# Performance work log

Hardware: AMD Instinct MI355X
Metric: run time of the kernel (lower is better)

Reference implementation:

```python
import jax, jax.numpy as jnp
import numpy as np

B, LQ, LK = 16, 256, 256
DQ = DK = DV = H = 256


def setup_inputs() -> dict:
    key = jax.random.key(0)
    ks = jax.random.split(key, 7)
    queries = jax.random.normal(ks[0], (B, LQ, DQ), dtype=jnp.float32)
    keys = jax.random.normal(ks[1], (B, LK, DK), dtype=jnp.float32)
    values = jax.random.normal(ks[2], (B, LK, DV), dtype=jnp.float32)
    valid_lens = jax.random.randint(ks[3], (B,), 1, LK + 1).astype(jnp.int32)
    W_q = jax.random.normal(ks[4], (DQ, H), dtype=jnp.float32) / np.sqrt(DQ)
    W_k = jax.random.normal(ks[5], (DK, H), dtype=jnp.float32) / np.sqrt(DK)
    w_v = jax.random.normal(ks[6], (H,), dtype=jnp.float32) / np.sqrt(H)
    return {"queries": queries, "keys": keys, "values": values,
            "valid_lens": valid_lens, "W_q": W_q, "W_k": W_k, "w_v": w_v}


def reference(queries, keys, values, valid_lens, W_q, W_k, w_v):
    # Project queries and keys to the hidden size (no bias)
    q = jnp.einsum('bqd,dh->bqh', queries, W_q)          # (B, Lq, H)
    k = jnp.einsum('bkd,dh->bkh', keys, W_k)             # (B, Lk, H)
    # Broadcast-add, tanh, then contract with w_v -> scores (B, Lq, Lk)
    features = jnp.tanh(q[:, :, None, :] + k[:, None, :, :])  # (B, Lq, Lk, H)
    scores = jnp.einsum('bqkh,h->bqk', features, w_v)
    # Masked softmax over last axis: positions >= valid_len get -1e6
    mask = jnp.arange(scores.shape[-1]) < valid_lens[:, None, None]  # (B,1,Lk) bcast
    scores = jnp.where(mask, scores, jnp.float32(-1e6))
    attn = jax.nn.softmax(scores, axis=-1)
    # Dropout is identity at inference (training=False)
    return jnp.einsum('bqk,bkv->bqv', attn, values)      # (B, Lq, Dv)
```

## Files before the change

### kernel.cpp

```cpp
#include <hip/hip_runtime.h>

using bf16x8 = __attribute__((ext_vector_type(8))) __bf16;
using f32x4  = __attribute__((ext_vector_type(4))) float;
using f32x2  = __attribute__((ext_vector_type(2))) float;
using us8    = __attribute__((ext_vector_type(8))) unsigned short;

#define TWO_LOG2E 2.8853900817779268f
#define LOG2E 1.4426950408889634f

__device__ __forceinline__ unsigned short f2bf(float x) {
  unsigned int u = __float_as_uint(x);
  u = (u + 0x7fffu + ((u >> 16) & 1u)) >> 16;
  return (unsigned short)u;
}
__device__ __forceinline__ float bf2f(unsigned short h) {
  return __uint_as_float(((unsigned int)h) << 16);
}
__device__ __forceinline__ f32x2 pk_fma(f32x2 a, f32x2 b, f32x2 c) {
  return __builtin_elementwise_fma(a, b, c);
}

__global__ __launch_bounds__(256) void tcast_kernel(
    const float* __restrict__ Wq, const float* __restrict__ Wk,
    const float* __restrict__ vals, const float* __restrict__ wv,
    unsigned short* __restrict__ wt_hi, unsigned short* __restrict__ wt_lo,
    unsigned short* __restrict__ vt_hi, unsigned short* __restrict__ vt_lo,
    float* __restrict__ wv2, float* __restrict__ Wsum) {
  if (blockIdx.x == 0) {
    int t = threadIdx.x;
    wv2[t] = -2.0f * wv[t];
    if (t < 64) {
      float s = wv[t] + wv[t + 64] + wv[t + 128] + wv[t + 192];
#pragma unroll
      for (int off = 1; off < 64; off <<= 1) s += __shfl_xor(s, off, 64);
      if (t == 0) Wsum[0] = s;
    }
  }
  __shared__ float tile[32][33];
  int m = blockIdx.x >> 6;
  int ts = blockIdx.x & 63;
  int R0 = (ts >> 3) << 5, C0 = (ts & 7) << 5;
  const float* src = (m == 0) ? Wq : (m == 1) ? Wk : (vals + ((m - 2) << 16));
  int r = threadIdx.x >> 3, c4 = (threadIdx.x & 7) << 2;
  float4 v = *(const float4*)(src + (R0 + r) * 256 + C0 + c4);
  tile[r][c4] = v.x; tile[r][c4 + 1] = v.y; tile[r][c4 + 2] = v.z; tile[r][c4 + 3] = v.w;
  __syncthreads();
  float o0 = tile[c4 + 0][r], o1 = tile[c4 + 1][r];
  float o2 = tile[c4 + 2][r], o3 = tile[c4 + 3][r];
  unsigned short h0 = f2bf(o0), h1 = f2bf(o1), h2 = f2bf(o2), h3 = f2bf(o3);
  int base = ((m < 2) ? (m << 16) : ((m - 2) << 16)) + (C0 + r) * 256 + R0 + c4;
  unsigned short* dh = (m < 2) ? wt_hi : vt_hi;
  unsigned short* dl = (m < 2) ? wt_lo : vt_lo;
  *(ushort4*)(dh + base) = make_ushort4(h0, h1, h2, h3);
  *(ushort4*)(dl + base) = make_ushort4(f2bf(o0 - bf2f(h0)), f2bf(o1 - bf2f(h1)),
                                        f2bf(o2 - bf2f(h2)), f2bf(o3 - bf2f(h3)));
}

__global__ __launch_bounds__(256, 4) void proj_kernel(
    const float* __restrict__ q, const float* __restrict__ kk,
    const unsigned short* __restrict__ w_hi, const unsigned short* __restrict__ w_lo,
    const int* __restrict__ vlens, float* __restrict__ Rq, float* __restrict__ RkT) {
  int wave = threadIdx.x >> 6, lane = threadIdx.x & 63;
  int mt = (blockIdx.x << 1) + (wave & 1);
  int m0 = mt << 4;
  int g = mt >> 8;
  if (g) {
    int bb = (m0 >> 8) & 15;
    if ((m0 & 255) >= vlens[bb]) return;
  }
  int r = lane & 15, qd = lane >> 4;
  int row = m0 + r;
  const float* A = (g == 0) ? (q + row * 256) : (kk + (row - 4096) * 256);
  bf16x8 ah[8], al[8];
#pragma unroll
  for (int s = 0; s < 8; ++s) {
    const float* p = A + qd * 8 + s * 32;
    float4 f0 = *(const float4*)p;
    float4 f1 = *(const float4*)(p + 4);
    float fv[8] = {f0.x, f0.y, f0.z, f0.w, f1.x, f1.y, f1.z, f1.w};
#pragma unroll
    for (int j = 0; j < 8; ++j) {
      __bf16 h = (__bf16)fv[j];
      ah[s][j] = h;
      al[s][j] = (__bf16)(fv[j] - (float)h);
    }
  }
  int nbase = (blockIdx.y << 6) + ((wave >> 1) << 5);
#pragma unroll
  for (int tI = 0; tI < 2; ++tI) {
    int n0 = nbase + (tI << 4);
    int boff = (g << 16) + (n0 + r) * 256 + qd * 8;
    f32x4 acc = {0.f, 0.f, 0.f, 0.f};
#pragma unroll
    for (int s = 0; s < 8; ++s) {
      bf16x8 bh = *(const bf16x8*)(w_hi + boff + s * 32);
      bf16x8 bl = *(const bf16x8*)(w_lo + boff + s * 32);
      acc = __builtin_amdgcn_mfma_f32_16x16x32_bf16(ah[s], bh, acc, 0, 0, 0);
      acc = __builtin_amdgcn_mfma_f32_16x16x32_bf16(ah[s], bl, acc, 0, 0, 0);
      acc = __builtin_amdgcn_mfma_f32_16x16x32_bf16(al[s], bh, acc, 0, 0, 0);
    }
    f32x4 ex;
#pragma unroll
    for (int i = 0; i < 4; ++i) {
      float l = acc[i] * TWO_LOG2E;
      l = fminf(fmaxf(l, -27.f), 27.f);
      ex[i] = __builtin_amdgcn_exp2f(l);
    }
    if (g == 0) {
#pragma unroll
      for (int i = 0; i < 4; ++i)
        Rq[(m0 + qd * 4 + i) * 256 + n0 + r] = ex[i];
    } else {
      int b = (m0 >> 8) & 15;
      int kloc = (m0 & 255) + qd * 4;
      *(f32x4*)(RkT + (b << 16) + (n0 + r) * 256 + kloc) = ex;
    }
  }
}

__global__ __launch_bounds__(256, 8) void scores_kernel(
    const float* __restrict__ Rq, const float* __restrict__ RkT,
    const float* __restrict__ wv2, const float* __restrict__ Wsum,
    const int* __restrict__ vlens, float* __restrict__ sc) {
  const int b = blockIdx.x;
  const int k0 = blockIdx.y << 5;
  const int vl = vlens[b];
  if (k0 >= vl) return;
  __shared__ __align__(16) float rqs[32 * 76];
  __shared__ __align__(16) float kT[64 * 34];
  const int t = threadIdx.x;
  const int q0 = blockIdx.z << 5;
  const int qrow = (b << 8) + q0;
  const int tq = t >> 4, tk = t & 15;
  const int sr = t >> 3, shb = (t & 7) << 3;
  const int hrow = t >> 2, kq = (t & 3) << 3;
  f32x2 a0 = {0.f, 0.f}, a1 = {0.f, 0.f};

  for (int hc = 0; hc < 4; ++hc) {
    if (hc) __syncthreads();
    const float* gq = Rq + (qrow + sr) * 256 + (hc << 6) + shb;
    *(float4*)(rqs + sr * 76 + shb)     = *(const float4*)gq;
    *(float4*)(rqs + sr * 76 + shb + 4) = *(const float4*)(gq + 4);
    const float* gk = RkT + (b << 16) + ((hc << 6) + hrow) * 256 + k0 + kq;
    *(float4*)(kT + hrow * 34 + kq)     = *(const float4*)gk;
    *(float4*)(kT + hrow * 34 + kq + 4) = *(const float4*)(gk + 4);
    __syncthreads();
#pragma unroll 2
    for (int h = 0; h < 64; h += 4) {
      f32x4 qa = *(const f32x4*)(rqs + tq * 76 + h);
      f32x4 qb = *(const f32x4*)(rqs + (tq + 16) * 76 + h);
      f32x4 wm = *(const f32x4*)(wv2 + (hc << 6) + h);
#pragma unroll
      for (int j = 0; j < 4; ++j) {
        f32x2 rk = *(const f32x2*)(kT + (h + j) * 34 + (tk << 1));
        f32x2 wj = (f32x2)(wm[j]);
        f32x2 d0 = pk_fma(rk, (f32x2)(qa[j]), (f32x2)(1.0f));
        f32x2 d1 = pk_fma(rk, (f32x2)(qb[j]), (f32x2)(1.0f));
        f32x2 r0, r1;
        r0.x = __uint_as_float(0x7EF311C3u - __float_as_uint(d0.x));
        r0.y = __uint_as_float(0x7EF311C3u - __float_as_uint(d0.y));
        r1.x = __uint_as_float(0x7EF311C3u - __float_as_uint(d1.x));
        r1.y = __uint_as_float(0x7EF311C3u - __float_as_uint(d1.y));
        r0 = r0 * pk_fma(-d0, r0, (f32x2)(2.0f));
        r1 = r1 * pk_fma(-d1, r1, (f32x2)(2.0f));
        a0 = pk_fma(r0, wj, a0);
        a1 = pk_fma(r1, wj, a1);
      }
    }
  }
  float ws = Wsum[0];
  a0 += (f32x2)(ws);
  a1 += (f32x2)(ws);
  *(f32x2*)(sc + ((qrow + tq) << 8) + k0 + (tk << 1)) = a0;
  *(f32x2*)(sc + ((qrow + tq + 16) << 8) + k0 + (tk << 1)) = a1;
}

__global__ __launch_bounds__(256) void av_fused_kernel(
    const float* __restrict__ sc, const int* __restrict__ vlens,
    const unsigned short* __restrict__ vhi, const unsigned short* __restrict__ vlo,
    float* __restrict__ out) {
  __shared__ __align__(16) unsigned short athi[16 * 264];
  const int wave = threadIdx.x >> 6, lane = threadIdx.x & 63;
  const int b = blockIdx.x;
  const int nh = blockIdx.y;
  const int m0 = blockIdx.z << 4;
  const int vl = vlens[b];

  {
    int row = (wave << 2) + (lane & 3);
    int c0 = (lane >> 2) << 4;
    const float* srow = sc + ((b << 8) + m0 + row) * 256 + c0;
    float4 x0 = *(const float4*)(srow);
    float4 x1 = *(const float4*)(srow + 4);
    float4 x2 = *(const float4*)(srow + 8);
    float4 x3 = *(const float4*)(srow + 12);
    float p[16] = {x0.x, x0.y, x0.z, x0.w, x1.x, x1.y, x1.z, x1.w,
                   x2.x, x2.y, x2.z, x2.w, x3.x, x3.y, x3.z, x3.w};
#pragma unroll
    for (int i = 0; i < 16; ++i)
      if (c0 + i >= vl) p[i] = -1e6f;
    float mx = p[0];
#pragma unroll
    for (int i = 1; i < 16; ++i) mx = fmaxf(mx, p[i]);
#pragma unroll
    for (int off = 4; off <= 32; off <<= 1) mx = fmaxf(mx, __shfl_xor(mx, off, 64));
    float sm = 0.f;
#pragma unroll
    for (int i = 0; i < 16; ++i) {
      p[i] = __builtin_amdgcn_exp2f((p[i] - mx) * LOG2E);
      sm += p[i];
    }
#pragma unroll
    for (int off = 4; off <= 32; off <<= 1) sm += __shfl_xor(sm, off, 64);
    float rs = __builtin_amdgcn_rcpf(sm);
    us8 vh[2];
#pragma unroll
    for (int i = 0; i < 16; ++i) vh[i >> 3][i & 7] = f2bf(p[i] * rs);
    *(us8*)(athi + row * 264 + c0)     = vh[0];
    *(us8*)(athi + row * 264 + c0 + 8) = vh[1];
  }
  __syncthreads();

  const int r = lane & 15, qd = lane >> 4;
  const int smax = (vl + 31) >> 5;
#pragma unroll
  for (int tI = 0; tI < 2; ++tI) {
    int n0 = (nh << 7) + (wave << 5) + (tI << 4);
    int boff = (b << 16) + (n0 + r) * 256 + qd * 8;
    f32x4 acc = {0.f, 0.f, 0.f, 0.f};
    for (int s = 0; s < smax; ++s) {
      bf16x8 ah = *(const bf16x8*)(athi + r * 264 + qd * 8 + s * 32);
      bf16x8 bh = *(const bf16x8*)(vhi + boff + s * 32);
      bf16x8 bl = *(const bf16x8*)(vlo + boff + s * 32);
      acc = __builtin_amdgcn_mfma_f32_16x16x32_bf16(ah, bh, acc, 0, 0, 0);
      acc = __builtin_amdgcn_mfma_f32_16x16x32_bf16(ah, bl, acc, 0, 0, 0);
    }
#pragma unroll
    for (int i = 0; i < 4; ++i)
      out[(b << 16) + (m0 + qd * 4 + i) * 256 + n0 + r] = acc[i];
  }
}

extern "C" void kernel_launch(void* const* d_in, const int* in_sizes, int n_in,
                              void* d_out, int out_size, void* d_ws, size_t ws_size,
                              hipStream_t stream) {
  const float* queries = (const float*)d_in[0];
  const float* keys    = (const float*)d_in[1];
  const float* values  = (const float*)d_in[2];
  const int*   vlens   = (const int*)d_in[3];
  const float* Wq      = (const float*)d_in[4];
  const float* Wk      = (const float*)d_in[5];
  const float* wv      = (const float*)d_in[6];
  float* out = (float*)d_out;
  char* ws = (char*)d_ws;

  unsigned short* wt_hi = (unsigned short*)(ws + 0);
  unsigned short* wt_lo = (unsigned short*)(ws + 262144);
  unsigned short* vt_hi = (unsigned short*)(ws + 524288);
  unsigned short* vt_lo = (unsigned short*)(ws + 2621440);
  float*          Rq    = (float*)(ws + 4718592);
  float*          RkT   = (float*)(ws + 8912896);
  float*          sc    = (float*)(ws + 13107200);
  float*          wv2   = (float*)(ws + 17301504);
  float*          Wsum  = (float*)(ws + 17302528);

  tcast_kernel<<<1152, 256, 0, stream>>>(Wq, Wk, values, wv,
                                         wt_hi, wt_lo, vt_hi, vt_lo, wv2, Wsum);
  proj_kernel<<<dim3(256, 4), 256, 0, stream>>>(queries, keys, wt_hi, wt_lo,
                                                vlens, Rq, RkT);
  scores_kernel<<<dim3(16, 8, 8), 256, 0, stream>>>(Rq, RkT, wv2, Wsum, vlens, sc);
  av_fused_kernel<<<dim3(16, 2, 16), 256, 0, stream>>>(sc, vlens, vt_hi, vt_lo, out);
}
```

Before: 139.4 us.

## Use persistent scores kernel with atomic work queue over valid tiles

Replaces the 3D scores grid, where blocks past valid_len exit early, with a persistent grid of 512 blocks. The blocks pull compacted (batch, k-tile, q-tile) items from a global atomic counter, using a prefix sum of per-batch tile counts built in tcast_kernel. This targets load imbalance and the cost of launching blocks that do no work under ragged valid lengths. It adds one atomic and two barriers per item, a linear search over batches, and depends on the counter being reset by the earlier kernel.

```diff
diff --git a/kernel.cpp b/kernel.cpp
--- a/kernel.cpp
+++ b/kernel.cpp
@@ -23,9 +23,11 @@
 __global__ __launch_bounds__(256) void tcast_kernel(
     const float* __restrict__ Wq, const float* __restrict__ Wk,
     const float* __restrict__ vals, const float* __restrict__ wv,
+    const int* __restrict__ vlens,
     unsigned short* __restrict__ wt_hi, unsigned short* __restrict__ wt_lo,
     unsigned short* __restrict__ vt_hi, unsigned short* __restrict__ vt_lo,
-    float* __restrict__ wv2, float* __restrict__ Wsum) {
+    float* __restrict__ wv2, float* __restrict__ Wsum,
+    int* __restrict__ ctr, int* __restrict__ cum) {
   if (blockIdx.x == 0) {
     int t = threadIdx.x;
     wv2[t] = -2.0f * wv[t];
@@ -34,6 +36,15 @@
 #pragma unroll
       for (int off = 1; off < 64; off <<= 1) s += __shfl_xor(s, off, 64);
       if (t == 0) Wsum[0] = s;
+    }
+    if (t == 0) {
+      ctr[0] = 0;
+      int c = 0;
+      for (int b = 0; b < 16; ++b) {
+        cum[b] = c;
+        c += ((vlens[b] + 31) >> 5) << 3;
+      }
+      cum[16] = c;
     }
   }
   __shared__ float tile[32][33];
@@ -121,58 +132,69 @@
 __global__ __launch_bounds__(256, 8) void scores_kernel(
     const float* __restrict__ Rq, const float* __restrict__ RkT,
     const float* __restrict__ wv2, const float* __restrict__ Wsum,
-    const int* __restrict__ vlens, float* __restrict__ sc) {
-  const int b = blockIdx.x;
-  const int k0 = blockIdx.y << 5;
-  const int vl = vlens[b];
-  if (k0 >= vl) return;
+    const int* __restrict__ cum, int* __restrict__ ctr,
+    float* __restrict__ sc) {
   __shared__ __align__(16) float rqs[32 * 76];
   __shared__ __align__(16) float kT[64 * 34];
+  __shared__ int s_item;
   const int t = threadIdx.x;
-  const int q0 = blockIdx.z << 5;
-  const int qrow = (b << 8) + q0;
   const int tq = t >> 4, tk = t & 15;
   const int sr = t >> 3, shb = (t & 7) << 3;
   const int hrow = t >> 2, kq = (t & 3) << 3;
-  f32x2 a0 = {0.f, 0.f}, a1 = {0.f, 0.f};
-
-  for (int hc = 0; hc < 4; ++hc) {
-    if (hc) __syncthreads();
-    const float* gq = Rq + (qrow + sr) * 256 + (hc << 6) + shb;
-    *(float4*)(rqs + sr * 76 + shb)     = *(const float4*)gq;
-    *(float4*)(rqs + sr * 76 + shb + 4) = *(const float4*)(gq + 4);
-    const float* gk = RkT + (b << 16) + ((hc << 6) + hrow) * 256 + k0 + kq;
-    *(float4*)(kT + hrow * 34 + kq)     = *(const float4*)gk;
-    *(float4*)(kT + hrow * 34 + kq + 4) = *(const float4*)(gk + 4);
+  const int total = cum[16];
+  const float ws = Wsum[0];
+
+  for (;;) {
     __syncthreads();
+    if (t == 0) s_item = atomicAdd(ctr, 1);
+    __syncthreads();
+    const int w = s_item;
+    if (w >= total) return;
+    int b = 0;
+    while (cum[b + 1] <= w) ++b;
+    const int local = w - cum[b];
+    const int k0 = (local >> 3) << 5;
+    const int q0 = (local & 7) << 5;
+    const int qrow = (b << 8) + q0;
+    f32x2 a0 = {0.f, 0.f}, a1 = {0.f, 0.f};
+
+    for (int hc = 0; hc < 4; ++hc) {
+      if (hc) __syncthreads();
+      const float* gq = Rq + (qrow + sr) * 256 + (hc << 6) + shb;
+      *(float4*)(rqs + sr * 76 + shb)     = *(const float4*)gq;
+      *(float4*)(rqs + sr * 76 + shb + 4) = *(const float4*)(gq + 4);
+      const float* gk = RkT + (b << 16) + ((hc << 6) + hrow) * 256 + k0 + kq;
+      *(float4*)(kT + hrow * 34 + kq)     = *(const float4*)gk;
+      *(float4*)(kT + hrow * 34 + kq + 4) = *(const float4*)(gk + 4);
+      __syncthreads();
 #pragma unroll 2
-    for (int h = 0; h < 64; h += 4) {
-      f32x4 qa = *(const f32x4*)(rqs + tq * 76 + h);
-      f32x4 qb = *(const f32x4*)(rqs + (tq + 16) * 76 + h);
-      f32x4 wm = *(const f32x4*)(wv2 + (hc << 6) + h);
-#pragma unroll
-      for (int j = 0; j < 4; ++j) {
-        f32x2 rk = *(const f32x2*)(kT + (h + j) * 34 + (tk << 1));
-        f32x2 wj = (f32x2)(wm[j]);
-        f32x2 d0 = pk_fma(rk, (f32x2)(qa[j]), (f32x2)(1.0f));
-        f32x2 d1 = pk_fma(rk, (f32x2)(qb[j]), (f32x2)(1.0f));
-        f32x2 r0, r1;
-        r0.x = __uint_as_float(0x7EF311C3u - __float_as_uint(d0.x));
-        r0.y = __uint_as_float(0x7EF311C3u - __float_as_uint(d0.y));
-        r1.x = __uint_as_float(0x7EF311C3u - __float_as_uint(d1.x));
-        r1.y = __uint_as_float(0x7EF311C3u - __float_as_uint(d1.y));
-        r0 = r0 * pk_fma(-d0, r0, (f32x2)(2.0f));
-        r1 = r1 * pk_fma(-d1, r1, (f32x2)(2.0f));
-        a0 = pk_fma(r0, wj, a0);
-        a1 = pk_fma(r1, wj, a1);
+      for (int h = 0; h < 64; h += 4) {
+        f32x4 qa = *(const f32x4*)(rqs + tq * 76 + h);
+        f32x4 qb = *(const f32x4*)(rqs + (tq + 16) * 76 + h);
+        f32x4 wm = *(const f32x4*)(wv2 + (hc << 6) + h);
+#pragma unroll
+        for (int j = 0; j < 4; ++j) {
+          f32x2 rk = *(const f32x2*)(kT + (h + j) * 34 + (tk << 1));
+          f32x2 wj = (f32x2)(wm[j]);
+          f32x2 d0 = pk_fma(rk, (f32x2)(qa[j]), (f32x2)(1.0f));
+          f32x2 d1 = pk_fma(rk, (f32x2)(qb[j]), (f32x2)(1.0f));
+          f32x2 r0, r1;
+          r0.x = __uint_as_float(0x7EF311C3u - __float_as_uint(d0.x));
+          r0.y = __uint_as_float(0x7EF311C3u - __float_as_uint(d0.y));
+          r1.x = __uint_as_float(0x7EF311C3u - __float_as_uint(d1.x));
+          r1.y = __uint_as_float(0x7EF311C3u - __float_as_uint(d1.y));
+          r0 = r0 * pk_fma(-d0, r0, (f32x2)(2.0f));
+          r1 = r1 * pk_fma(-d1, r1, (f32x2)(2.0f));
+          a0 = pk_fma(r0, wj, a0);
+          a1 = pk_fma(r1, wj, a1);
+        }
       }
     }
-  }
-  float ws = Wsum[0];
-  a0 += (f32x2)(ws);
-  a1 += (f32x2)(ws);
-  *(f32x2*)(sc + ((qrow + tq) << 8) + k0 + (tk << 1)) = a0;
-  *(f32x2*)(sc + ((qrow + tq + 16) << 8) + k0 + (tk << 1)) = a1;
+    a0 += (f32x2)(ws);
+    a1 += (f32x2)(ws);
+    *(f32x2*)(sc + ((qrow + tq) << 8) + k0 + (tk << 1)) = a0;
+    *(f32x2*)(sc + ((qrow + tq + 16) << 8) + k0 + (tk << 1)) = a1;
+  }
 }
 
 __global__ __launch_bounds__(256) void av_fused_kernel(
@@ -263,11 +285,14 @@
   float*          sc    = (float*)(ws + 13107200);
   float*          wv2   = (float*)(ws + 17301504);
   float*          Wsum  = (float*)(ws + 17302528);
-
-  tcast_kernel<<<1152, 256, 0, stream>>>(Wq, Wk, values, wv,
-                                         wt_hi, wt_lo, vt_hi, vt_lo, wv2, Wsum);
+  int*            ctr   = (int*)(ws + 17302532);
+  int*            cum   = (int*)(ws + 17302536);
+
+  tcast_kernel<<<1152, 256, 0, stream>>>(Wq, Wk, values, wv, vlens,
+                                         wt_hi, wt_lo, vt_hi, vt_lo, wv2, Wsum,
+                                         ctr, cum);
   proj_kernel<<<dim3(256, 4), 256, 0, stream>>>(queries, keys, wt_hi, wt_lo,
                                                 vlens, Rq, RkT);
-  scores_kernel<<<dim3(16, 8, 8), 256, 0, stream>>>(Rq, RkT, wv2, Wsum, vlens, sc);
+  scores_kernel<<<512, 256, 0, stream>>>(Rq, RkT, wv2, Wsum, cum, ctr, sc);
   av_fused_kernel<<<dim3(16, 2, 16), 256, 0, stream>>>(sc, vlens, vt_hi, vt_lo, out);
 }
```

After: 135.5 us. 2.8% less time.
